# Optimization experiments

Hardware: AMD Instinct MI355X
Metric: run time of the kernel (lower is better)

Reference implementation:

```python
import jax, jax.numpy as jnp
import numpy as np

N_NODES = 100000
N_EDGES = 1600000
N_GRAPHS = 512
F_IN = 20
HID = 128
OUT = HID // 2


def _glorot(key, shape):
    fan_in, fan_out = shape[0], shape[1]
    lim = float(np.sqrt(6.0 / (fan_in + fan_out)))
    return jax.random.uniform(key, shape, jnp.float32, -lim, lim)


def setup_inputs() -> dict:
    key = jax.random.key(0)
    ks = jax.random.split(key, 12)
    x = jax.random.normal(ks[0], (N_NODES, F_IN), jnp.float32)
    edge_index = jax.random.randint(ks[1], (2, N_EDGES), 0, N_NODES, dtype=jnp.int64)
    batch = jnp.sort(jax.random.randint(ks[2], (N_NODES,), 0, N_GRAPHS, dtype=jnp.int64))
    return {
        "x": x,
        "edge_index": edge_index,
        "batch": batch,
        "W1": _glorot(ks[3], (F_IN, HID)), "b1": jnp.zeros((HID,), jnp.float32),
        "W2": _glorot(ks[4], (HID, HID)), "b2": jnp.zeros((HID,), jnp.float32),
        "W3": _glorot(ks[5], (HID, HID)), "b3": jnp.zeros((HID,), jnp.float32),
        "Wout": _glorot(ks[6], (HID, OUT)), "bout": jnp.zeros((OUT,), jnp.float32),
    }


def _gcn_conv(x, W, b, src, dst, num_nodes):
    # PyG GCNConv: x' = D^{-1/2} (A + I) D^{-1/2} X W + b (self-loops already in src/dst)
    xw = x @ W                                                  # [N, H]
    ones = jnp.ones(src.shape[0], dtype=xw.dtype)
    deg = jax.ops.segment_sum(ones, dst, num_segments=num_nodes)
    dinv = jnp.where(deg > 0, jax.lax.rsqrt(deg), 0.0)          # [N]
    norm = dinv[src] * dinv[dst]                                # [E+N]
    msg = xw[src] * norm[:, None]                               # gather + scale
    return jax.ops.segment_sum(msg, dst, num_segments=num_nodes) + b


def reference(x, edge_index, batch, W1, b1, W2, b2, W3, b3, Wout, bout):
    num_nodes = x.shape[0]
    loops = jnp.arange(num_nodes, dtype=edge_index.dtype)
    src = jnp.concatenate([edge_index[0], loops])
    dst = jnp.concatenate([edge_index[1], loops])

    h = jax.nn.relu(_gcn_conv(x, W1, b1, src, dst, num_nodes))
    h = jax.nn.relu(_gcn_conv(h, W2, b2, src, dst, num_nodes))
    h = jax.nn.relu(_gcn_conv(h, W3, b3, src, dst, num_nodes))

    # global_mean_pool over graph ids
    sums = jax.ops.segment_sum(h, batch, num_segments=N_GRAPHS)
    counts = jax.ops.segment_sum(jnp.ones(num_nodes, h.dtype), batch, num_segments=N_GRAPHS)
    pooled = sums / jnp.maximum(counts, 1.0)[:, None]           # [G, H]
    return pooled @ Wout + bout                                 # [G, H//2]
```

## Files before the change

### kernel.cpp

```cpp
#include <hip/hip_runtime.h>
#include <hip/hip_fp16.h>

#define N_NODES 100000
#define N_EDGES 1600000
#define N_GRAPHS 512
#define F_IN 20
#define HID 128
#define OUT_F 64

#define BUCKETS 512
#define SPAN 196
#define BCAP 3500
#define EPB 4096

typedef _Float16 half8_t __attribute__((ext_vector_type(8)));
typedef float f32x4_t __attribute__((ext_vector_type(4)));

__device__ inline float4 h4_to_f4(uint2 u) {
    __half2 h0 = *(__half2*)&u.x;
    __half2 h1 = *(__half2*)&u.y;
    float2 f0 = __half22float2(h0);
    float2 f1 = __half22float2(h1);
    return make_float4(f0.x, f0.y, f1.x, f1.y);
}

__global__ __launch_bounds__(512) void partition(const int* __restrict__ src,
                                                 const int* __restrict__ dst,
                                                 int* __restrict__ bpairs,
                                                 int* cur512) {
    __shared__ int lcnt[8][BUCKETS];
    __shared__ int woff[8][BUCKETS];
    int t = threadIdx.x;
    int wv = t >> 6;
    for (int i = t; i < 8 * BUCKETS; i += 512) ((int*)lcnt)[i] = 0;
    __syncthreads();
    int base = blockIdx.x * EPB;
    int myb[8], myp[8], myr[8];
#pragma unroll
    for (int i = 0; i < 8; ++i) {
        int e = base + i * 512 + t;
        int b = -1, p = 0, rk = 0;
        if (e < N_EDGES) {
            int s = src[e], d = dst[e];
            b = d / SPAN;
            p = (s << 9) | (d - b * SPAN);
            rk = atomicAdd(&lcnt[wv][b], 1);
        }
        myb[i] = b; myp[i] = p; myr[i] = rk;
    }
    __syncthreads();
    {
        int c[8], tot = 0;
#pragma unroll
        for (int w = 0; w < 8; ++w) { c[w] = lcnt[w][t]; tot += c[w]; }
        int gb = atomicAdd(&cur512[t], tot);
#pragma unroll
        for (int w = 0; w < 8; ++w) { woff[w][t] = gb; gb += c[w]; }
    }
    __syncthreads();
#pragma unroll
    for (int i = 0; i < 8; ++i) {
        int b = myb[i];
        if (b >= 0) {
            int p = woff[wv][b] + myr[i];
            if (p < BCAP) bpairs[(size_t)b * BCAP + p] = myp[i];
        }
    }
}

__global__ __launch_bounds__(512) void csr_build(const int* __restrict__ bpairs,
                                                 const int* __restrict__ cur512,
                                                 int* __restrict__ row_st,
                                                 int* __restrict__ csr,
                                                 const float* __restrict__ x,
                                                 __half* __restrict__ Xs) {
    __shared__ int ocnt[SPAN];
    __shared__ int sc[512];
    __shared__ int cur[SPAN];
    __shared__ int sbase;
    int b = blockIdx.x, t = threadIdx.x;

    int myc = cur512[t];
    sc[t] = myc;
    __syncthreads();
    for (int o = 1; o < BUCKETS; o <<= 1) {
        int v = (t >= o) ? sc[t - o] : 0;
        __syncthreads();
        sc[t] += v;
        __syncthreads();
    }
    if (t == b) sbase = sc[t] - myc;
    if (b == BUCKETS - 1 && t == 0) row_st[N_NODES] = N_EDGES;

    int n0 = b * SPAN;
    int span = N_NODES - n0; if (span > SPAN) span = SPAN;
    if (span < 0) span = 0;
    if (t < SPAN) ocnt[t] = 0;
    __syncthreads();

    int n = cur512[b];
    if (n > BCAP) n = BCAP;
    const int* p = bpairs + (size_t)b * BCAP;
    for (int i = t; i < n; i += 512) atomicAdd(&ocnt[p[i] & 511], 1);
    __syncthreads();
    sc[t] = (t < span) ? ocnt[t] : 0;
    __syncthreads();
    for (int o = 1; o < 512; o <<= 1) {
        int v = (t >= o) ? sc[t - o] : 0;
        __syncthreads();
        sc[t] += v;
        __syncthreads();
    }
    int base = sbase;
    if (t < span) {
        int start = sc[t] - ocnt[t];
        row_st[n0 + t] = base + start;
        cur[t] = start;
    }
    __syncthreads();
    for (int i = t; i < n; i += 512) {
        int e = p[i];
        int lp = atomicAdd(&cur[e & 511], 1);
        csr[base + lp] = e >> 9;
    }
    for (int i = t; i < span * 32; i += 512) {
        int nl = i >> 5, f = i & 31;
        float v = (f < F_IN) ? x[(size_t)(n0 + nl) * F_IN + f] : 0.f;
        float di = rsqrtf((float)(ocnt[nl] + 1));
        Xs[(size_t)(n0 + nl) * 32 + f] = __float2half(di * v);
    }
}

__global__ __launch_bounds__(256) void layer1(const __half* __restrict__ Xs,
                                              const int* __restrict__ row_st,
                                              const int* __restrict__ csr,
                                              const float* __restrict__ W,
                                              const float* __restrict__ bias,
                                              __half* __restrict__ H) {
    __shared__ float Wlds[F_IN * HID];
    __shared__ float Alds[16 * F_IN];
    const int t = threadIdx.x;
    const int node0 = blockIdx.x * 16;

    for (int i = t; i < F_IN * HID; i += 256) Wlds[i] = W[i];

    const int h16 = t >> 4;
    const int l16 = t & 15;
    const __half2* X2 = (const __half2*)Xs;
    {
        int nn = node0 + h16;
        int r0 = row_st[nn], r1 = row_st[nn + 1];
        float2 f = __half22float2(X2[(size_t)nn * 16 + l16]);
        float2 acc = f;
        int r = r0;
        for (; r + 1 < r1; r += 2) {
            float2 f0 = __half22float2(X2[(size_t)csr[r] * 16 + l16]);
            float2 f1 = __half22float2(X2[(size_t)csr[r + 1] * 16 + l16]);
            acc.x += f0.x + f1.x;
            acc.y += f0.y + f1.y;
        }
        if (r < r1) {
            float2 f2 = __half22float2(X2[(size_t)csr[r] * 16 + l16]);
            acc.x += f2.x; acc.y += f2.y;
        }
        if (l16 < 10) {
            float di = rsqrtf((float)(r1 - r0 + 1));
            Alds[h16 * F_IN + l16 * 2]     = di * acc.x;
            Alds[h16 * F_IN + l16 * 2 + 1] = di * acc.y;
        }
    }
    __syncthreads();

    const int g  = t >> 5;
    const int h4 = (t & 31) * 4;
    float4 b4 = *(const float4*)&bias[h4];
    float4 acc0 = b4;
    float4 acc1 = b4;
#pragma unroll
    for (int kk = 0; kk < F_IN; ++kk) {
        float a0 = Alds[(g * 2) * F_IN + kk];
        float a1 = Alds[(g * 2 + 1) * F_IN + kk];
        float4 w = *(const float4*)&Wlds[kk * HID + h4];
        acc0.x = fmaf(a0, w.x, acc0.x);
        acc0.y = fmaf(a0, w.y, acc0.y);
        acc0.z = fmaf(a0, w.z, acc0.z);
        acc0.w = fmaf(a0, w.w, acc0.w);
        acc1.x = fmaf(a1, w.x, acc1.x);
        acc1.y = fmaf(a1, w.y, acc1.y);
        acc1.z = fmaf(a1, w.z, acc1.z);
        acc1.w = fmaf(a1, w.w, acc1.w);
    }
    {
        __half2 h0 = __floats2half2_rn(acc0.x, acc0.y);
        __half2 h1 = __floats2half2_rn(acc0.z, acc0.w);
        uint2 u; u.x = *(unsigned*)&h0; u.y = *(unsigned*)&h1;
        ((uint2*)H)[(node0 + g * 2) * 32 + (h4 >> 2)] = u;
    }
    {
        __half2 h0 = __floats2half2_rn(acc1.x, acc1.y);
        __half2 h1 = __floats2half2_rn(acc1.z, acc1.w);
        uint2 u; u.x = *(unsigned*)&h0; u.y = *(unsigned*)&h1;
        ((uint2*)H)[(node0 + g * 2 + 1) * 32 + (h4 >> 2)] = u;
    }
}

__global__ __launch_bounds__(256) void gemm_mfma(const __half* __restrict__ H,
                                                 const float* __restrict__ W,
                                                 const int* __restrict__ row_st,
                                                 __half* __restrict__ T) {
    __shared__ _Float16 Whi[64 * 128];
    __shared__ _Float16 Wlo[64 * 128];
    const int t = threadIdx.x;
    const int c0 = (blockIdx.x & 1) * 64;

    for (int i = t; i < 128 * 64; i += 256) {
        int k = i >> 6, c = i & 63;
        float w = W[k * HID + c0 + c];
        _Float16 hi = (_Float16)w;
        _Float16 lo = (_Float16)((w - (float)hi) * 2048.0f);
        int addr = c * 128 + (((k >> 3) ^ (c & 15)) << 3) + (k & 7);
        Whi[addr] = hi;
        Wlo[addr] = lo;
    }
    __syncthreads();

    const int wv = t >> 6;
    const int l  = t & 63;
    const int lr = l & 15;
    const int lq = l >> 4;

    for (int rep = 0; rep < 4; ++rep) {
        int strip = ((blockIdx.x >> 1) * 4 + wv) * 4 + rep;
        if (strip >= N_NODES / 16) continue;
        int n0 = strip * 16;

        f32x4_t acc[4], acl[4];
#pragma unroll
        for (int ct = 0; ct < 4; ++ct) { acc[ct] = (f32x4_t){0,0,0,0}; acl[ct] = (f32x4_t){0,0,0,0}; }

#pragma unroll
        for (int kc = 0; kc < 4; ++kc) {
            half8_t a = *(const half8_t*)(H + (size_t)(n0 + lr) * 128 + kc * 32 + lq * 8);
#pragma unroll
            for (int j = 0; j < 8; ++j) a[j] = a[j] > (_Float16)0 ? a[j] : (_Float16)0;
            int g = kc * 4 + lq;
#pragma unroll
            for (int ct = 0; ct < 4; ++ct) {
                int c = ct * 16 + lr;
                int addr = c * 128 + ((g ^ lr) << 3);
                half8_t bh = *(const half8_t*)&Whi[addr];
                half8_t bl = *(const half8_t*)&Wlo[addr];
                acc[ct] = __builtin_amdgcn_mfma_f32_16x16x32_f16(a, bh, acc[ct], 0, 0, 0);
                acl[ct] = __builtin_amdgcn_mfma_f32_16x16x32_f16(a, bl, acl[ct], 0, 0, 0);
            }
        }

        int r0 = n0 + lq * 4;
#pragma unroll
        for (int r = 0; r < 4; ++r) {
            int row = r0 + r;
            float d = rsqrtf((float)(row_st[row + 1] - row_st[row] + 1));
#pragma unroll
            for (int ct = 0; ct < 4; ++ct) {
                float v = (acc[ct][r] + acl[ct][r] * 4.8828125e-4f) * d;
                T[(size_t)row * 128 + c0 + ct * 16 + lr] = __float2half(v);
            }
        }
    }
}

__global__ __launch_bounds__(256) void gather_range(const __half* __restrict__ A,
                                                    const int* __restrict__ row_st,
                                                    const int* __restrict__ csr,
                                                    const float* __restrict__ bias,
                                                    __half* __restrict__ B) {
    int t = threadIdx.x;
    int n = blockIdx.x * 8 + (t >> 5);
    int l = t & 31;
    int r0 = row_st[n], r1 = row_st[n + 1];
    float di = rsqrtf((float)(r1 - r0 + 1));
    const uint2* Af = (const uint2*)A;
    float4 acc = h4_to_f4(Af[n * 32 + l]);
    int r = r0;
    for (; r + 7 < r1; r += 8) {
        int s0 = csr[r],     s1 = csr[r + 1], s2 = csr[r + 2], s3 = csr[r + 3];
        int s4 = csr[r + 4], s5 = csr[r + 5], s6 = csr[r + 6], s7 = csr[r + 7];
        float4 v0 = h4_to_f4(Af[s0 * 32 + l]);
        float4 v1 = h4_to_f4(Af[s1 * 32 + l]);
        float4 v2 = h4_to_f4(Af[s2 * 32 + l]);
        float4 v3 = h4_to_f4(Af[s3 * 32 + l]);
        float4 v4 = h4_to_f4(Af[s4 * 32 + l]);
        float4 v5 = h4_to_f4(Af[s5 * 32 + l]);
        float4 v6 = h4_to_f4(Af[s6 * 32 + l]);
        float4 v7 = h4_to_f4(Af[s7 * 32 + l]);
        acc.x += ((v0.x + v1.x) + (v2.x + v3.x)) + ((v4.x + v5.x) + (v6.x + v7.x));
        acc.y += ((v0.y + v1.y) + (v2.y + v3.y)) + ((v4.y + v5.y) + (v6.y + v7.y));
        acc.z += ((v0.z + v1.z) + (v2.z + v3.z)) + ((v4.z + v5.z) + (v6.z + v7.z));
        acc.w += ((v0.w + v1.w) + (v2.w + v3.w)) + ((v4.w + v5.w) + (v6.w + v7.w));
    }
    for (; r + 3 < r1; r += 4) {
        int s0 = csr[r], s1 = csr[r + 1], s2 = csr[r + 2], s3 = csr[r + 3];
        float4 v0 = h4_to_f4(Af[s0 * 32 + l]);
        float4 v1 = h4_to_f4(Af[s1 * 32 + l]);
        float4 v2 = h4_to_f4(Af[s2 * 32 + l]);
        float4 v3 = h4_to_f4(Af[s3 * 32 + l]);
        acc.x += (v0.x + v1.x) + (v2.x + v3.x);
        acc.y += (v0.y + v1.y) + (v2.y + v3.y);
        acc.z += (v0.z + v1.z) + (v2.z + v3.z);
        acc.w += (v0.w + v1.w) + (v2.w + v3.w);
    }
    for (; r < r1; ++r) {
        float4 v = h4_to_f4(Af[csr[r] * 32 + l]);
        acc.x += v.x; acc.y += v.y; acc.z += v.z; acc.w += v.w;
    }
    float4 b4 = ((const float4*)bias)[l];
    __half2 h0 = __floats2half2_rn(fmaf(di, acc.x, b4.x), fmaf(di, acc.y, b4.y));
    __half2 h1 = __floats2half2_rn(fmaf(di, acc.z, b4.z), fmaf(di, acc.w, b4.w));
    uint2 u; u.x = *(unsigned*)&h0; u.y = *(unsigned*)&h1;
    ((uint2*)B)[n * 32 + l] = u;
}

__global__ __launch_bounds__(256) void pool_head(const __half* __restrict__ H,
                                                 const int* __restrict__ batch,
                                                 const float* __restrict__ Wout,
                                                 const float* __restrict__ bout,
                                                 float* __restrict__ out) {
    __shared__ float4 part[8][32];
    __shared__ float p[HID];
    __shared__ int bounds[2];
    int g = blockIdx.x;
    int t = threadIdx.x;
    if (t < 2) {
        int target = g + t;
        int lo = 0, hi = N_NODES;
        while (lo < hi) {
            int mid = (lo + hi) >> 1;
            if (batch[mid] < target) lo = mid + 1; else hi = mid;
        }
        bounds[t] = lo;
    }
    __syncthreads();
    int lo = bounds[0], hi = bounds[1];
    int grp = t >> 5, l = t & 31;
    const uint2* Hf = (const uint2*)H;
    float4 acc = make_float4(0.f, 0.f, 0.f, 0.f);
    for (int n = lo + grp; n < hi; n += 8) {
        float4 v = h4_to_f4(Hf[(size_t)n * 32 + l]);
        acc.x += fmaxf(v.x, 0.f);
        acc.y += fmaxf(v.y, 0.f);
        acc.z += fmaxf(v.z, 0.f);
        acc.w += fmaxf(v.w, 0.f);
    }
    part[grp][l] = acc;
    __syncthreads();
    if (t < 32) {
        float4 s = part[0][t];
#pragma unroll
        for (int j = 1; j < 8; ++j) {
            float4 v = part[j][t];
            s.x += v.x; s.y += v.y; s.z += v.z; s.w += v.w;
        }
        float inv = 1.0f / fmaxf((float)(hi - lo), 1.0f);
        p[t * 4 + 0] = s.x * inv;
        p[t * 4 + 1] = s.y * inv;
        p[t * 4 + 2] = s.z * inv;
        p[t * 4 + 3] = s.w * inv;
    }
    __syncthreads();
    if (t < OUT_F) {
        float acc2 = 0.f;
#pragma unroll 8
        for (int k = 0; k < HID; ++k)
            acc2 = fmaf(p[k], Wout[k * OUT_F + t], acc2);
        out[g * OUT_F + t] = acc2 + bout[t];
    }
}

extern "C" void kernel_launch(void* const* d_in, const int* in_sizes, int n_in,
                              void* d_out, int out_size, void* d_ws, size_t ws_size,
                              hipStream_t stream) {
    const float* x     = (const float*)d_in[0];
    const int*   ei    = (const int*)d_in[1];
    const int*   batch = (const int*)d_in[2];
    const float* W1    = (const float*)d_in[3];
    const float* b1    = (const float*)d_in[4];
    const float* W2    = (const float*)d_in[5];
    const float* b2    = (const float*)d_in[6];
    const float* W3    = (const float*)d_in[7];
    const float* b3    = (const float*)d_in[8];
    const float* Wout  = (const float*)d_in[9];
    const float* bout  = (const float*)d_in[10];
    float* out = (float*)d_out;

    const int* src = ei;
    const int* dst = ei + N_EDGES;

    float* A      = (float*)d_ws;
    float* Breg   = A + (size_t)N_NODES * HID;
    int*   row_st = (int*)(Breg + (size_t)N_NODES * HID);
    int*   cur512 = row_st + N_NODES + 1;
    int*   csr    = cur512 + BUCKETS;

    int*    bpairs = (int*)A;
    __half* Xs     = (__half*)((char*)A + 7168000);
    __half* T      = (__half*)A;
    __half* H      = (__half*)Breg;

    hipMemsetAsync(cur512, 0, BUCKETS * sizeof(int), stream);
    partition<<<(N_EDGES + EPB - 1) / EPB, 512, 0, stream>>>(src, dst, bpairs, cur512);
    csr_build<<<BUCKETS, 512, 0, stream>>>(bpairs, cur512, row_st, csr, x, Xs);

    layer1<<<N_NODES / 16, 256, 0, stream>>>(Xs, row_st, csr, W1, b1, H);

    gemm_mfma<<<782, 256, 0, stream>>>(H, W2, row_st, T);
    gather_range<<<N_NODES / 8, 256, 0, stream>>>(T, row_st, csr, b2, H);
    gemm_mfma<<<782, 256, 0, stream>>>(H, W3, row_st, T);
    gather_range<<<N_NODES / 8, 256, 0, stream>>>(T, row_st, csr, b3, H);

    pool_head<<<N_GRAPHS, 256, 0, stream>>>(H, batch, Wout, bout, out);
}
```

Measured before the change: 352.7 us.

## Store hidden features as four column slices and gather per slice

Hidden-feature buffers now use a sliced layout, four slices of 32 columns each, contiguous per node, and every kernel that touches them is updated. The gather kernel processes one 32-column slice per block, interleaving slices across adjacent blocks. The aim is a smaller working set per gather pass, so the randomly gathered source rows fit better in cache. CSR index loads and the output stores become nontemporal. The cost is four passes over the CSR indices per layer, and 64-byte gather granules instead of 256-byte ones. A stray label statement was also added.

```diff
diff --git a/kernel.cpp b/kernel.cpp
--- a/kernel.cpp
+++ b/kernel.cpp
@@ -188,19 +188,22 @@
         acc1.x = fmaf(a1, w.x, acc1.x);
         acc1.y = fmaf(a1, w.y, acc1.y);
         acc1.z = fmaf(a1, w.z, acc1.z);
+        ac1:
         acc1.w = fmaf(a1, w.w, acc1.w);
     }
+    const size_t sl = (size_t)(h4 >> 5) * N_NODES;
+    const int wi = (h4 >> 2) & 7;
     {
         __half2 h0 = __floats2half2_rn(acc0.x, acc0.y);
         __half2 h1 = __floats2half2_rn(acc0.z, acc0.w);
         uint2 u; u.x = *(unsigned*)&h0; u.y = *(unsigned*)&h1;
-        ((uint2*)H)[(node0 + g * 2) * 32 + (h4 >> 2)] = u;
+        ((uint2*)H)[(sl + node0 + g * 2) * 8 + wi] = u;
     }
     {
         __half2 h0 = __floats2half2_rn(acc1.x, acc1.y);
         __half2 h1 = __floats2half2_rn(acc1.z, acc1.w);
         uint2 u; u.x = *(unsigned*)&h0; u.y = *(unsigned*)&h1;
-        ((uint2*)H)[(node0 + g * 2 + 1) * 32 + (h4 >> 2)] = u;
+        ((uint2*)H)[(sl + node0 + g * 2 + 1) * 8 + wi] = u;
     }
 }
 
@@ -240,7 +243,7 @@
 
 #pragma unroll
         for (int kc = 0; kc < 4; ++kc) {
-            half8_t a = *(const half8_t*)(H + (size_t)(n0 + lr) * 128 + kc * 32 + lq * 8);
+            half8_t a = *(const half8_t*)(H + ((size_t)kc * N_NODES + n0 + lr) * 32 + lq * 8);
 #pragma unroll
             for (int j = 0; j < 8; ++j) a[j] = a[j] > (_Float16)0 ? a[j] : (_Float16)0;
             int g = kc * 4 + lq;
@@ -263,61 +266,80 @@
 #pragma unroll
             for (int ct = 0; ct < 4; ++ct) {
                 float v = (acc[ct][r] + acl[ct][r] * 4.8828125e-4f) * d;
-                T[(size_t)row * 128 + c0 + ct * 16 + lr] = __float2half(v);
+                int c = c0 + ct * 16 + lr;
+                T[((size_t)(c >> 5) * N_NODES + row) * 32 + (c & 31)] = __float2half(v);
             }
         }
     }
 }
 
-__global__ __launch_bounds__(256) void gather_range(const __half* __restrict__ A,
+__global__ __launch_bounds__(256) void gather_slice(const __half* __restrict__ T,
                                                     const int* __restrict__ row_st,
                                                     const int* __restrict__ csr,
                                                     const float* __restrict__ bias,
                                                     __half* __restrict__ B) {
     int t = threadIdx.x;
-    int n = blockIdx.x * 8 + (t >> 5);
-    int l = t & 31;
+    int b = blockIdx.x;
+    int x = b & 7;
+    int slice = x >> 1;
+    int chunk = (b >> 3) * 2 + (x & 1);
+    int grp = t >> 3;
+    int l   = t & 7;
+    int n = chunk * 32 + grp;
+    if (n >= N_NODES) return;
     int r0 = row_st[n], r1 = row_st[n + 1];
     float di = rsqrtf((float)(r1 - r0 + 1));
-    const uint2* Af = (const uint2*)A;
-    float4 acc = h4_to_f4(Af[n * 32 + l]);
+    const uint2* Tf = (const uint2*)T + (size_t)slice * N_NODES * 8;
+    float4 acc = h4_to_f4(Tf[(size_t)n * 8 + l]);
     int r = r0;
     for (; r + 7 < r1; r += 8) {
-        int s0 = csr[r],     s1 = csr[r + 1], s2 = csr[r + 2], s3 = csr[r + 3];
-        int s4 = csr[r + 4], s5 = csr[r + 5], s6 = csr[r + 6], s7 = csr[r + 7];
-        float4 v0 = h4_to_f4(Af[s0 * 32 + l]);
-        float4 v1 = h4_to_f4(Af[s1 * 32 + l]);
-        float4 v2 = h4_to_f4(Af[s2 * 32 + l]);
-        float4 v3 = h4_to_f4(Af[s3 * 32 + l]);
-        float4 v4 = h4_to_f4(Af[s4 * 32 + l]);
-        float4 v5 = h4_to_f4(Af[s5 * 32 + l]);
-        float4 v6 = h4_to_f4(Af[s6 * 32 + l]);
-        float4 v7 = h4_to_f4(Af[s7 * 32 + l]);
+        int s0 = __builtin_nontemporal_load(csr + r);
+        int s1 = __builtin_nontemporal_load(csr + r + 1);
+        int s2 = __builtin_nontemporal_load(csr + r + 2);
+        int s3 = __builtin_nontemporal_load(csr + r + 3);
+        int s4 = __builtin_nontemporal_load(csr + r + 4);
+        int s5 = __builtin_nontemporal_load(csr + r + 5);
+        int s6 = __builtin_nontemporal_load(csr + r + 6);
+        int s7 = __builtin_nontemporal_load(csr + r + 7);
+        float4 v0 = h4_to_f4(Tf[(size_t)s0 * 8 + l]);
+        float4 v1 = h4_to_f4(Tf[(size_t)s1 * 8 + l]);
+        float4 v2 = h4_to_f4(Tf[(size_t)s2 * 8 + l]);
+        float4 v3 = h4_to_f4(Tf[(size_t)s3 * 8 + l]);
+        float4 v4 = h4_to_f4(Tf[(size_t)s4 * 8 + l]);
+        float4 v5 = h4_to_f4(Tf[(size_t)s5 * 8 + l]);
+        float4 v6 = h4_to_f4(Tf[(size_t)s6 * 8 + l]);
+        float4 v7 = h4_to_f4(Tf[(size_t)s7 * 8 + l]);
         acc.x += ((v0.x + v1.x) + (v2.x + v3.x)) + ((v4.x + v5.x) + (v6.x + v7.x));
         acc.y += ((v0.y + v1.y) + (v2.y + v3.y)) + ((v4.y + v5.y) + (v6.y + v7.y));
         acc.z += ((v0.z + v1.z) + (v2.z + v3.z)) + ((v4.z + v5.z) + (v6.z + v7.z));
         acc.w += ((v0.w + v1.w) + (v2.w + v3.w)) + ((v4.w + v5.w) + (v6.w + v7.w));
     }
     for (; r + 3 < r1; r += 4) {
-        int s0 = csr[r], s1 = csr[r + 1], s2 = csr[r + 2], s3 = csr[r + 3];
-        float4 v0 = h4_to_f4(Af[s0 * 32 + l]);
-        float4 v1 = h4_to_f4(Af[s1 * 32 + l]);
-        float4 v2 = h4_to_f4(Af[s2 * 32 + l]);
-        float4 v3 = h4_to_f4(Af[s3 * 32 + l]);
+        int s0 = __builtin_nontemporal_load(csr + r);
+        int s1 = __builtin_nontemporal_load(csr + r + 1);
+        int s2 = __builtin_nontemporal_load(csr + r + 2);
+        int s3 = __builtin_nontemporal_load(csr + r + 3);
+        float4 v0 = h4_to_f4(Tf[(size_t)s0 * 8 + l]);
+        float4 v1 = h4_to_f4(Tf[(size_t)s1 * 8 + l]);
+        float4 v2 = h4_to_f4(Tf[(size_t)s2 * 8 + l]);
+        float4 v3 = h4_to_f4(Tf[(size_t)s3 * 8 + l]);
         acc.x += (v0.x + v1.x) + (v2.x + v3.x);
         acc.y += (v0.y + v1.y) + (v2.y + v3.y);
         acc.z += (v0.z + v1.z) + (v2.z + v3.z);
         acc.w += (v0.w + v1.w) + (v2.w + v3.w);
     }
     for (; r < r1; ++r) {
-        float4 v = h4_to_f4(Af[csr[r] * 32 + l]);
+        int s0 = __builtin_nontemporal_load(csr + r);
+        float4 v = h4_to_f4(Tf[(size_t)s0 * 8 + l]);
         acc.x += v.x; acc.y += v.y; acc.z += v.z; acc.w += v.w;
     }
-    float4 b4 = ((const float4*)bias)[l];
+    float4 b4 = ((const float4*)bias)[slice * 8 + l];
     __half2 h0 = __floats2half2_rn(fmaf(di, acc.x, b4.x), fmaf(di, acc.y, b4.y));
     __half2 h1 = __floats2half2_rn(fmaf(di, acc.z, b4.z), fmaf(di, acc.w, b4.w));
-    uint2 u; u.x = *(unsigned*)&h0; u.y = *(unsigned*)&h1;
-    ((uint2*)B)[n * 32 + l] = u;
+    unsigned lo = *(unsigned*)&h0, hi = *(unsigned*)&h1;
+    unsigned long long uv = ((unsigned long long)hi << 32) | lo;
+    unsigned long long* dst = (unsigned long long*)((uint2*)B + ((size_t)slice * N_NODES + n) * 8 + l);
+    __builtin_nontemporal_store(uv, dst);
 }
 
 __global__ __launch_bounds__(256) void pool_head(const __half* __restrict__ H,
@@ -344,8 +366,10 @@
     int grp = t >> 5, l = t & 31;
     const uint2* Hf = (const uint2*)H;
     float4 acc = make_float4(0.f, 0.f, 0.f, 0.f);
+    const size_t sbase = (size_t)(l >> 3) * N_NODES;
+    const int wi = l & 7;
     for (int n = lo + grp; n < hi; n += 8) {
-        float4 v = h4_to_f4(Hf[(size_t)n * 32 + l]);
+        float4 v = h4_to_f4(Hf[(sbase + n) * 8 + wi]);
         acc.x += fmaxf(v.x, 0.f);
         acc.y += fmaxf(v.y, 0.f);
         acc.z += fmaxf(v.z, 0.f);
@@ -413,9 +437,9 @@
     layer1<<<N_NODES / 16, 256, 0, stream>>>(Xs, row_st, csr, W1, b1, H);
 
     gemm_mfma<<<782, 256, 0, stream>>>(H, W2, row_st, T);
-    gather_range<<<N_NODES / 8, 256, 0, stream>>>(T, row_st, csr, b2, H);
+    gather_slice<<<12504, 256, 0, stream>>>(T, row_st, csr, b2, H);
     gemm_mfma<<<782, 256, 0, stream>>>(H, W3, row_st, T);
-    gather_range<<<N_NODES / 8, 256, 0, stream>>>(T, row_st, csr, b3, H);
+    gather_slice<<<12504, 256, 0, stream>>>(T, row_st, csr, b3, H);
 
     pool_head<<<N_GRAPHS, 256, 0, stream>>>(H, batch, Wout, bout, out);
 }
```

Result: slower. 421.8 us (+19.6%).

## Split node features into two 64-wide slices to shrink gather working set

Applied to the files above, without the earlier changes.

Stores the fp16 hidden features as two column slices, each a [N,64] array, instead of one interleaved [N,128] array. Layer1, the MFMA GEMM and pooling are all updated to read and write this layout. The gather kernel now gives each block one slice, with blocks interleaved so the two slices of neighbouring node chunks run close together. The goal is a smaller random-gather footprint per pass (6.4MB per slice) that fits better in L2/MALL, at the cost of reading the CSR indices twice. Output stores are also made nontemporal.

```diff
diff --git a/kernel.cpp b/kernel.cpp
--- a/kernel.cpp
+++ b/kernel.cpp
@@ -190,17 +190,19 @@
         acc1.z = fmaf(a1, w.z, acc1.z);
         acc1.w = fmaf(a1, w.w, acc1.w);
     }
+    const size_t sl = (size_t)((t & 31) >> 4) * N_NODES;
+    const int wi = t & 15;
     {
         __half2 h0 = __floats2half2_rn(acc0.x, acc0.y);
         __half2 h1 = __floats2half2_rn(acc0.z, acc0.w);
         uint2 u; u.x = *(unsigned*)&h0; u.y = *(unsigned*)&h1;
-        ((uint2*)H)[(node0 + g * 2) * 32 + (h4 >> 2)] = u;
+        ((uint2*)H)[(sl + node0 + g * 2) * 16 + wi] = u;
     }
     {
         __half2 h0 = __floats2half2_rn(acc1.x, acc1.y);
         __half2 h1 = __floats2half2_rn(acc1.z, acc1.w);
         uint2 u; u.x = *(unsigned*)&h0; u.y = *(unsigned*)&h1;
-        ((uint2*)H)[(node0 + g * 2 + 1) * 32 + (h4 >> 2)] = u;
+        ((uint2*)H)[(sl + node0 + g * 2 + 1) * 16 + wi] = u;
     }
 }
 
@@ -240,7 +242,8 @@
 
 #pragma unroll
         for (int kc = 0; kc < 4; ++kc) {
-            half8_t a = *(const half8_t*)(H + (size_t)(n0 + lr) * 128 + kc * 32 + lq * 8);
+            half8_t a = *(const half8_t*)(H + ((size_t)(kc >> 1) * N_NODES + n0 + lr) * 64
+                                            + (kc & 1) * 32 + lq * 8);
 #pragma unroll
             for (int j = 0; j < 8; ++j) a[j] = a[j] > (_Float16)0 ? a[j] : (_Float16)0;
             int g = kc * 4 + lq;
@@ -263,36 +266,42 @@
 #pragma unroll
             for (int ct = 0; ct < 4; ++ct) {
                 float v = (acc[ct][r] + acl[ct][r] * 4.8828125e-4f) * d;
-                T[(size_t)row * 128 + c0 + ct * 16 + lr] = __float2half(v);
+                int c = c0 + ct * 16 + lr;
+                T[((size_t)(c >> 6) * N_NODES + row) * 64 + (c & 63)] = __float2half(v);
             }
         }
     }
 }
 
-__global__ __launch_bounds__(256) void gather_range(const __half* __restrict__ A,
-                                                    const int* __restrict__ row_st,
-                                                    const int* __restrict__ csr,
-                                                    const float* __restrict__ bias,
-                                                    __half* __restrict__ B) {
+__global__ __launch_bounds__(256) void gather_half(const __half* __restrict__ T,
+                                                   const int* __restrict__ row_st,
+                                                   const int* __restrict__ csr,
+                                                   const float* __restrict__ bias,
+                                                   __half* __restrict__ B) {
     int t = threadIdx.x;
-    int n = blockIdx.x * 8 + (t >> 5);
-    int l = t & 31;
+    int b = blockIdx.x;
+    int x = b & 7;
+    int slice = x >> 2;
+    int chunk = (b >> 3) * 4 + (x & 3);
+    int n = chunk * 16 + (t >> 4);
+    int l = t & 15;
+    if (n >= N_NODES) return;
     int r0 = row_st[n], r1 = row_st[n + 1];
     float di = rsqrtf((float)(r1 - r0 + 1));
-    const uint2* Af = (const uint2*)A;
-    float4 acc = h4_to_f4(Af[n * 32 + l]);
+    const uint2* Tf = (const uint2*)T + (size_t)slice * N_NODES * 16;
+    float4 acc = h4_to_f4(Tf[(size_t)n * 16 + l]);
     int r = r0;
     for (; r + 7 < r1; r += 8) {
         int s0 = csr[r],     s1 = csr[r + 1], s2 = csr[r + 2], s3 = csr[r + 3];
         int s4 = csr[r + 4], s5 = csr[r + 5], s6 = csr[r + 6], s7 = csr[r + 7];
-        float4 v0 = h4_to_f4(Af[s0 * 32 + l]);
-        float4 v1 = h4_to_f4(Af[s1 * 32 + l]);
-        float4 v2 = h4_to_f4(Af[s2 * 32 + l]);
-        float4 v3 = h4_to_f4(Af[s3 * 32 + l]);
-        float4 v4 = h4_to_f4(Af[s4 * 32 + l]);
-        float4 v5 = h4_to_f4(Af[s5 * 32 + l]);
-        float4 v6 = h4_to_f4(Af[s6 * 32 + l]);
-        float4 v7 = h4_to_f4(Af[s7 * 32 + l]);
+        float4 v0 = h4_to_f4(Tf[(size_t)s0 * 16 + l]);
+        float4 v1 = h4_to_f4(Tf[(size_t)s1 * 16 + l]);
+        float4 v2 = h4_to_f4(Tf[(size_t)s2 * 16 + l]);
+        float4 v3 = h4_to_f4(Tf[(size_t)s3 * 16 + l]);
+        float4 v4 = h4_to_f4(Tf[(size_t)s4 * 16 + l]);
+        float4 v5 = h4_to_f4(Tf[(size_t)s5 * 16 + l]);
+        float4 v6 = h4_to_f4(Tf[(size_t)s6 * 16 + l]);
+        float4 v7 = h4_to_f4(Tf[(size_t)s7 * 16 + l]);
         acc.x += ((v0.x + v1.x) + (v2.x + v3.x)) + ((v4.x + v5.x) + (v6.x + v7.x));
         acc.y += ((v0.y + v1.y) + (v2.y + v3.y)) + ((v4.y + v5.y) + (v6.y + v7.y));
         acc.z += ((v0.z + v1.z) + (v2.z + v3.z)) + ((v4.z + v5.z) + (v6.z + v7.z));
@@ -300,24 +309,26 @@
     }
     for (; r + 3 < r1; r += 4) {
         int s0 = csr[r], s1 = csr[r + 1], s2 = csr[r + 2], s3 = csr[r + 3];
-        float4 v0 = h4_to_f4(Af[s0 * 32 + l]);
-        float4 v1 = h4_to_f4(Af[s1 * 32 + l]);
-        float4 v2 = h4_to_f4(Af[s2 * 32 + l]);
-        float4 v3 = h4_to_f4(Af[s3 * 32 + l]);
+        float4 v0 = h4_to_f4(Tf[(size_t)s0 * 16 + l]);
+        float4 v1 = h4_to_f4(Tf[(size_t)s1 * 16 + l]);
+        float4 v2 = h4_to_f4(Tf[(size_t)s2 * 16 + l]);
+        float4 v3 = h4_to_f4(Tf[(size_t)s3 * 16 + l]);
         acc.x += (v0.x + v1.x) + (v2.x + v3.x);
         acc.y += (v0.y + v1.y) + (v2.y + v3.y);
         acc.z += (v0.z + v1.z) + (v2.z + v3.z);
         acc.w += (v0.w + v1.w) + (v2.w + v3.w);
     }
     for (; r < r1; ++r) {
-        float4 v = h4_to_f4(Af[csr[r] * 32 + l]);
+        float4 v = h4_to_f4(Tf[(size_t)csr[r] * 16 + l]);
         acc.x += v.x; acc.y += v.y; acc.z += v.z; acc.w += v.w;
     }
-    float4 b4 = ((const float4*)bias)[l];
+    float4 b4 = ((const float4*)bias)[slice * 16 + l];
     __half2 h0 = __floats2half2_rn(fmaf(di, acc.x, b4.x), fmaf(di, acc.y, b4.y));
     __half2 h1 = __floats2half2_rn(fmaf(di, acc.z, b4.z), fmaf(di, acc.w, b4.w));
-    uint2 u; u.x = *(unsigned*)&h0; u.y = *(unsigned*)&h1;
-    ((uint2*)B)[n * 32 + l] = u;
+    unsigned lo = *(unsigned*)&h0, hi = *(unsigned*)&h1;
+    unsigned long long uv = ((unsigned long long)hi << 32) | lo;
+    unsigned long long* dstp = (unsigned long long*)((uint2*)B + ((size_t)slice * N_NODES + n) * 16 + l);
+    __builtin_nontemporal_store(uv, dstp);
 }
 
 __global__ __launch_bounds__(256) void pool_head(const __half* __restrict__ H,
@@ -344,8 +355,10 @@
     int grp = t >> 5, l = t & 31;
     const uint2* Hf = (const uint2*)H;
     float4 acc = make_float4(0.f, 0.f, 0.f, 0.f);
+    const size_t sbase = (size_t)(l >> 4) * N_NODES;
+    const int wi = l & 15;
     for (int n = lo + grp; n < hi; n += 8) {
-        float4 v = h4_to_f4(Hf[(size_t)n * 32 + l]);
+        float4 v = h4_to_f4(Hf[(sbase + n) * 16 + wi]);
         acc.x += fmaxf(v.x, 0.f);
         acc.y += fmaxf(v.y, 0.f);
         acc.z += fmaxf(v.z, 0.f);
@@ -413,9 +426,9 @@
     layer1<<<N_NODES / 16, 256, 0, stream>>>(Xs, row_st, csr, W1, b1, H);
 
     gemm_mfma<<<782, 256, 0, stream>>>(H, W2, row_st, T);
-    gather_range<<<N_NODES / 8, 256, 0, stream>>>(T, row_st, csr, b2, H);
+    gather_half<<<12504, 256, 0, stream>>>(T, row_st, csr, b2, H);
     gemm_mfma<<<782, 256, 0, stream>>>(H, W3, row_st, T);
-    gather_range<<<N_NODES / 8, 256, 0, stream>>>(T, row_st, csr, b3, H);
+    gather_half<<<12504, 256, 0, stream>>>(T, row_st, csr, b3, H);
 
     pool_head<<<N_GRAPHS, 256, 0, stream>>>(H, batch, Wout, bout, out);
 }
```

New measurement: 362.6 us. +2.8%, slower.
